# Kernel optimization log

Measured on AMD Instinct MI355X. Metric: run time of the kernel, lower is better.

The kernel has to match this reference:

```python
import jax, jax.numpy as jnp
import numpy as np
from jax import lax

N, L, LQ = 1024, 120, 30
V, D = 50000, 200
POSV, P = 201, 5
H, R = 230, 96
BAG = 8
B = N // BAG
EMB = 3 * D + 2 * P  # 610


def setup_inputs() -> dict:
    key = jax.random.key(0)
    k = jax.random.split(key, 14)
    X = jax.random.randint(k[0], (N, L), 0, V, dtype=jnp.int32)
    Q = jax.random.randint(k[1], (N, LQ), 0, V, dtype=jnp.int32)
    X_Pos1 = jax.random.randint(k[2], (N, L), 0, POSV, dtype=jnp.int32)
    X_Pos2 = jax.random.randint(k[3], (N, L), 0, POSV, dtype=jnp.int32)
    starts = jnp.arange(B, dtype=jnp.int32) * BAG
    X_Scope = jnp.stack([starts, starts + BAG], axis=1)  # [B,2] bag boundaries
    X_Rel = jax.random.randint(k[4], (B,), 0, R, dtype=jnp.int32)
    word_emb = jax.random.normal(k[5], (V, D), jnp.float32) * 0.02
    pos1_emb = jax.random.normal(k[6], (POSV, P), jnp.float32) * 0.02
    pos2_emb = jax.random.normal(k[7], (POSV, P), jnp.float32) * 0.02
    ws_w = jax.random.normal(k[8], (D,), jnp.float32) * 0.05
    wq_w = jax.random.normal(k[9], (D,), jnp.float32) * 0.05
    wsq_w = jax.random.normal(k[10], (D,), jnp.float32) * 0.05
    conv_w = jax.random.normal(k[11], (H, EMB, 3), jnp.float32) * 0.02
    rel_w = jax.random.normal(k[12], (R, H), jnp.float32) * 0.05
    return {
        'X': X, 'Q': Q, 'X_Pos1': X_Pos1, 'X_Pos2': X_Pos2,
        'X_Scope': X_Scope, 'X_Rel': X_Rel,
        'word_emb': word_emb, 'pos1_emb': pos1_emb, 'pos2_emb': pos2_emb,
        'ws_w': ws_w, 'ws_b': jnp.zeros((), jnp.float32),
        'wq_w': wq_w, 'wq_b': jnp.zeros((), jnp.float32),
        'wsq_w': wsq_w, 'wsq_b': jnp.zeros((), jnp.float32),
        'conv_w': conv_w, 'conv_b': jnp.zeros((H,), jnp.float32),
        'rel_w': rel_w, 'rel_b': jnp.zeros((R,), jnp.float32),
    }


def _forward(X, Q, X_Pos1, X_Pos2, X_Scope, X_Rel, word_emb, pos1_emb, pos2_emb,
             ws_w, ws_b, wq_w, wq_b, wsq_w, wsq_b, conv_w, conv_b, rel_w, rel_b):
    s = word_emb[X]            # [N,L,D]
    q = word_emb[Q]            # [N,LQ,D]
    p1 = pos1_emb[X_Pos1]      # [N,L,P]
    p2 = pos2_emb[X_Pos2]
    # ---- qs_att (BiDAF-style), vectorized over the original per-q-position loop ----
    sq = jnp.einsum('nld,nqd,d->nlq', s, q, wsq_w) + wsq_b            # [N,L,LQ]
    h = (s @ ws_w + ws_b)[:, :, None] + (q @ wq_w + wq_b)[:, None, :] + sq
    a = jax.nn.softmax(h, axis=2)
    s2q = jnp.einsum('nlq,nqd->nld', a, q)                            # s2q_att
    bvec = jax.nn.softmax(jnp.max(h, axis=2), axis=1)                 # [N,L]
    q2s = jnp.einsum('nl,nld->nd', bvec, s)[:, None, :]               # [N,1,D]
    x = jnp.concatenate([s, s * s2q, s * q2s], axis=-1)               # [N,L,3D]
    x = jnp.concatenate([x, p1, p2], axis=-1)                         # [N,L,EMB]
    # ---- CNN encoder: conv1d(k=3, same) -> max-over-time -> relu ----
    xc = lax.conv_general_dilated(x.transpose(0, 2, 1), conv_w, (1,), 'SAME',
                                  dimension_numbers=('NCH', 'OIH', 'NCH'))
    xc = xc + conv_b[None, :, None]
    feat = jax.nn.relu(jnp.max(xc, axis=2))                           # [N,H]
    # ---- bag self-attention: per-bag scaled dot-product over sentences ----
    bag_id = jnp.searchsorted(X_Scope[:, 1], jnp.arange(feat.shape[0]), side='right')
    same = bag_id[:, None] == bag_id[None, :]
    scores = (feat @ feat.T) / jnp.sqrt(jnp.float32(feat.shape[-1]))
    scores = jnp.where(same, scores, -1e30)
    feat = jax.nn.softmax(scores, axis=-1) @ feat                     # [N,H]
    # ---- selective attention with gold relation query (segment softmax) ----
    relq = rel_w[X_Rel]                                               # [B,H]
    z = jnp.einsum('nh,nh->n', feat, relq[bag_id])
    m = jax.ops.segment_max(z, bag_id, num_segments=B)
    e = jnp.exp(z - m[bag_id])
    denom = jax.ops.segment_sum(e, bag_id, num_segments=B)
    w = e / denom[bag_id]
    bag_rep = jax.ops.segment_sum(w[:, None] * feat, bag_id, num_segments=B)
    return bag_rep @ rel_w.T + rel_b                                  # [B,R]


def reference(X, Q, X_Pos1, X_Pos2, X_Scope, X_Rel, word_emb, pos1_emb, pos2_emb,
              ws_w, ws_b, wq_w, wq_b, wsq_w, wsq_b, conv_w, conv_b, rel_w, rel_b):
    return _forward(X, Q, X_Pos1, X_Pos2, X_Scope, X_Rel, word_emb, pos1_emb, pos2_emb,
                    ws_w, ws_b, wq_w, wq_b, wsq_w, wsq_b, conv_w, conv_b, rel_w, rel_b)
```

## Files before the change

kernel.cpp:

```cpp
#include <hip/hip_runtime.h>
#include <hip/hip_bf16.h>

#define N_    1024
#define L_    120
#define LQ_   30
#define D_    200
#define P_    5
#define H_    230
#define R_    96
#define BAG_  8
#define B_    128
#define EMB_  610
#define SROWS 130
#define SSTR  232
#define XSTR  72
#define NCH   21

typedef __hip_bfloat16 bf16;
typedef __attribute__((ext_vector_type(8))) short short8;
typedef __attribute__((ext_vector_type(4))) short short4_;
typedef __attribute__((ext_vector_type(4))) float f32x4;

__device__ __forceinline__ float wred_sum64(float v) {
#pragma unroll
  for (int m = 32; m; m >>= 1) v += __shfl_xor(v, m, 64);
  return v;
}
__device__ __forceinline__ float wred_max64(float v) {
#pragma unroll
  for (int m = 32; m; m >>= 1) v = fmaxf(v, __shfl_xor(v, m, 64));
  return v;
}
__device__ __forceinline__ short f2b(float f) {
  bf16 h = __float2bfloat16(f);
  return __builtin_bit_cast(short, h);
}
__device__ __forceinline__ float b2f(bf16 h) { return __bfloat162float(h); }

__global__ __launch_bounds__(256) void k0_prep_w(
    const float* __restrict__ conv_w, bf16* __restrict__ wt)
{
  const int idx = blockIdx.x * 256 + threadIdx.x;
  int e = idx & 7, lane = (idx >> 3) & 63;
  int fid = idx >> 9;
  int ni = fid & 15, cb = (fid >> 4) % NCH, k = fid / (NCH * 16);
  int h = ni * 16 + (lane & 15);
  int ccl = ((lane >> 4) << 3) + e;
  float v = 0.f;
  if (h < H_) {
    int emb_c = -1;
    if (cb < 7) {
      int d = cb * 32 + ccl;
      if (d < D_) emb_c = d;
    } else if (cb < 20) {
      int t = cb - 7;
      int d = 16 * t + (ccl & 15);
      if (d < D_) emb_c = (ccl < 16) ? (D_ + d) : (2 * D_ + d);
    } else if (ccl < 2 * P_) {
      emb_c = 3 * D_ + ccl;
    }
    if (emb_c >= 0) v = conv_w[(size_t)h * (EMB_ * 3) + emb_c * 3 + k];
  }
  wt[idx] = __float2bfloat16(v);
}

__global__ __launch_bounds__(1024, 4) void kf_fused(
    const int* __restrict__ X, const int* __restrict__ Q,
    const int* __restrict__ P1, const int* __restrict__ P2,
    const float* __restrict__ word_emb,
    const float* __restrict__ pos1_emb, const float* __restrict__ pos2_emb,
    const float* __restrict__ ws_w, const float* __restrict__ ws_b,
    const float* __restrict__ wq_w, const float* __restrict__ wq_b,
    const float* __restrict__ wsq_w,
    const bf16* __restrict__ wt, const float* __restrict__ conv_b,
    float* __restrict__ feat)
{
  const int n = blockIdx.x;
  const int tid = threadIdx.x;
  const int w = tid >> 6, lane = tid & 63;
  const int g = lane >> 4, c = lane & 15;
  const int wm = w >> 3;
  const int wn = w & 7;
  const int w8 = w & 7;

  __shared__ __align__(16) bf16 s_lds[SROWS][SSTR];
  __shared__ __align__(16) bf16 qT[208][40];
  __shared__ __align__(16) bf16 a_bf[128][40];
  __shared__ __align__(16) bf16 xstage[2][SROWS][XSTR];
  __shared__ __align__(16) bf16 pos_lds[L_][10];
  __shared__ float hred[16][32];
  __shared__ float wsv[D_], wqv[D_], wsqv[D_];
  __shared__ float sdot[128], qdot[32], hmax[128], bvec[L_];
  __shared__ float q2p[4][D_];
  __shared__ int xidxs[L_], qidxs[LQ_];

  bf16 (*qsw)[SSTR] = (bf16(*)[SSTR])&xstage[0][0][0];

  {
    const int4 z4 = {0, 0, 0, 0};
    for (int t = tid; t < SROWS * SSTR * 2 / 16; t += 1024) ((int4*)s_lds)[t] = z4;
    for (int t = tid; t < 208 * 40 * 2 / 16;     t += 1024) ((int4*)qT)[t] = z4;
    for (int t = tid; t < 32 * SSTR * 2 / 16;    t += 1024) ((int4*)qsw)[t] = z4;
  }
  if (tid < 2) qdot[30 + tid] = 0.f;
  if (tid >= 120 && tid < 128) sdot[tid] = 0.f;
  for (int t = tid; t < D_; t += 1024) { wsv[t] = ws_w[t]; wqv[t] = wq_w[t]; wsqv[t] = wsq_w[t]; }
  if (tid < L_) xidxs[tid] = X[n * L_ + tid];
  else if (tid >= 128 && tid < 128 + LQ_) qidxs[tid - 128] = Q[n * LQ_ + (tid - 128)];
  __syncthreads();

  const float wsb = ws_b[0], wqb = wq_b[0];

  for (int l = w; l < L_; l += 16) {
    const int idx = xidxs[l];
    if (lane < 50) {
      const int d = lane * 4;
      float4 v = *(const float4*)(word_emb + (size_t)idx * D_ + d);
      short4_ pk; pk.x = f2b(v.x); pk.y = f2b(v.y); pk.z = f2b(v.z); pk.w = f2b(v.w);
      *(short4_*)&s_lds[1 + l][d] = pk;
    }
  }
  for (int e = tid; e < L_ * 10; e += 1024) {
    int r = e / 10, p = e % 10;
    float v = (p < P_) ? pos1_emb[(size_t)P1[n * L_ + r] * P_ + p]
                       : pos2_emb[(size_t)P2[n * L_ + r] * P_ + (p - P_)];
    pos_lds[r][p] = __float2bfloat16(v);
  }
  for (int j = w; j < LQ_; j += 16) {
    const int idx = qidxs[j];
    float part = 0.f;
    if (lane < 50) {
      const int d = lane * 4;
      float4 v = *(const float4*)(word_emb + (size_t)idx * D_ + d);
      part = v.x * wqv[d] + v.y * wqv[d + 1] + v.z * wqv[d + 2] + v.w * wqv[d + 3];
      short4_ pk;
      pk.x = f2b(v.x * wsqv[d]);     pk.y = f2b(v.y * wsqv[d + 1]);
      pk.z = f2b(v.z * wsqv[d + 2]); pk.w = f2b(v.w * wsqv[d + 3]);
      *(short4_*)&qsw[j][d] = pk;
      qT[d][j]     = __float2bfloat16(v.x);
      qT[d + 1][j] = __float2bfloat16(v.y);
      qT[d + 2][j] = __float2bfloat16(v.z);
      qT[d + 3][j] = __float2bfloat16(v.w);
    }
    float sum = wred_sum64(part);
    if (lane == 0) qdot[j] = sum + wqb;
  }
  __syncthreads();

  f32x4 acc0 = {0.f, 0.f, 0.f, 0.f}, acc1 = {0.f, 0.f, 0.f, 0.f};
  if (w < 8) {
#pragma unroll
    for (int kk = 0; kk < 7; ++kk) {
      short8 af = *(const short8*)&s_lds[1 + 16 * w + c][kk * 32 + g * 8];
      short8 b0 = *(const short8*)&qsw[c][kk * 32 + g * 8];
      short8 b1 = *(const short8*)&qsw[16 + c][kk * 32 + g * 8];
      acc0 = __builtin_amdgcn_mfma_f32_16x16x32_bf16(af, b0, acc0, 0, 0, 0);
      acc1 = __builtin_amdgcn_mfma_f32_16x16x32_bf16(af, b1, acc1, 0, 0, 0);
    }
  } else {
    const int idx = tid - 512;
    if (idx < 480) {
      const int r = idx >> 2, base = (idx & 3) * 50;
      float a = 0.f;
#pragma unroll 5
      for (int i = 0; i < 50; i += 2) {
        a += b2f(s_lds[1 + r][base + i]) * wsv[base + i];
        a += b2f(s_lds[1 + r][base + i + 1]) * wsv[base + i + 1];
      }
      a += __shfl_xor(a, 1, 64);
      a += __shfl_xor(a, 2, 64);
      if ((idx & 3) == 0) sdot[r] = a + wsb;
    }
  }
  __syncthreads();

  if (w < 8) {
    const int rbase = 16 * w + 4 * g;
    const float qd0 = qdot[c], qd1 = qdot[16 + c];
#pragma unroll
    for (int reg = 0; reg < 4; ++reg) {
      const int r = rbase + reg;
      const float s0 = sdot[r];
      float h0 = acc0[reg] + s0 + qd0;
      float h1 = (c < 14) ? (acc1[reg] + s0 + qd1) : -1e30f;
      float m = fmaxf(h0, h1);
#pragma unroll
      for (int msk = 1; msk < 16; msk <<= 1) m = fmaxf(m, __shfl_xor(m, msk, 64));
      float e0 = expf(h0 - m);
      float e1 = (c < 14) ? expf(h1 - m) : 0.f;
      float ssum = e0 + e1;
#pragma unroll
      for (int msk = 1; msk < 16; msk <<= 1) ssum += __shfl_xor(ssum, msk, 64);
      float inv = 1.f / ssum;
      a_bf[r][c]      = __float2bfloat16(e0 * inv);
      a_bf[r][16 + c] = __float2bfloat16(e1 * inv);
      if (c == 0) hmax[r] = m;
    }
  } else {
    const int4 z4 = {0, 0, 0, 0};
    for (int t = tid - 512; t < 2 * SROWS * XSTR * 2 / 16; t += 512) ((int4*)xstage)[t] = z4;
  }
  __syncthreads();

  if (w == 0) {
    float v0 = hmax[lane];
    float v1 = (lane < L_ - 64) ? hmax[64 + lane] : -1e30f;
    float m = wred_max64(fmaxf(v0, v1));
    float e0 = expf(v0 - m);
    float e1 = (lane < L_ - 64) ? expf(v1 - m) : 0.f;
    float inv = 1.f / wred_sum64(e0 + e1);
    bvec[lane] = e0 * inv;
    if (lane < L_ - 64) bvec[64 + lane] = e1 * inv;
  }
  __syncthreads();

  {
    const int d = tid & 255, quarter = tid >> 8;
    if (d < D_) {
      const int lb = quarter * 30;
      float a0 = 0.f, a1 = 0.f;
      for (int l = 0; l < 30; l += 2) {
        a0 += bvec[lb + l]     * b2f(s_lds[1 + lb + l][d]);
        a1 += bvec[lb + l + 1] * b2f(s_lds[1 + lb + l + 1][d]);
      }
      q2p[quarter][d] = a0 + a1;
    }
  }
  __syncthreads();

  const short* wts = (const short*)wt;
  const short8 aft = *(const short8*)&a_bf[16 * w8 + c][g * 8];

  f32x4 acc[4][2];
#pragma unroll
  for (int i = 0; i < 4; ++i) {
    acc[i][0] = (f32x4){0.f, 0.f, 0.f, 0.f};
    acc[i][1] = (f32x4){0.f, 0.f, 0.f, 0.f};
  }

  for (int p = 0; p < 7; ++p) {
    {
      const int t = 2 * p + wm;
      bf16 (*buf)[XSTR] = xstage[p & 1];
      if (t < 13) {
        short8 bfr = *(const short8*)&qT[t * 16 + c][g * 8];
        f32x4 o = __builtin_amdgcn_mfma_f32_16x16x32_bf16(aft, bfr, (f32x4){0.f,0.f,0.f,0.f}, 0, 0, 0);
#pragma unroll
        for (int reg = 0; reg < 4; ++reg) {
          const int r = 16 * w8 + 4 * g + reg;
          if (r < L_) {
            float sv = b2f(s_lds[1 + r][t * 16 + c]);
            buf[1 + r][(t & 1) * 32 + c] = __float2bfloat16(sv * o[reg]);
          }
        }
        for (int e = tid & 511; e < L_ * 16; e += 512) {
          const int row = e >> 4, cc = e & 15, dd = t * 16 + cc;
          float v = (dd < D_)
              ? b2f(s_lds[1 + row][dd]) * (q2p[0][dd] + q2p[1][dd] + q2p[2][dd] + q2p[3][dd])
              : 0.f;
          buf[1 + row][(t & 1) * 32 + 16 + cc] = __float2bfloat16(v);
        }
      } else {
        for (int e = tid & 511; e < SROWS * 32; e += 512) {
          const int r = e >> 5, cc = e & 31;
          bf16 v = __float2bfloat16(0.f);
          if (r >= 1 && r <= L_ && cc < 2 * P_) v = pos_lds[r - 1][cc];
          buf[r][32 + cc] = v;
        }
      }
    }

#pragma unroll
    for (int k = 0; k < 3; ++k) {
      short8 bx0 = *(const short8*)(
          wts + (((size_t)((k * NCH + p) * 16 + wn * 2 + 0)) << 9) + lane * 8);
      short8 bx1 = *(const short8*)(
          wts + (((size_t)((k * NCH + p) * 16 + wn * 2 + 1)) << 9) + lane * 8);
#pragma unroll
      for (int mi = 0; mi < 4; ++mi) {
        short8 af = *(const short8*)&s_lds[wm * 64 + mi * 16 + c + k][p * 32 + g * 8];
        acc[mi][0] = __builtin_amdgcn_mfma_f32_16x16x32_bf16(af, bx0, acc[mi][0], 0, 0, 0);
        acc[mi][1] = __builtin_amdgcn_mfma_f32_16x16x32_bf16(af, bx1, acc[mi][1], 0, 0, 0);
      }
    }
    __syncthreads();

    {
      bf16 (*buf)[XSTR] = xstage[p & 1];
#pragma unroll
      for (int s2 = 0; s2 < 2; ++s2) {
        const int t = 2 * p + s2;
        const int cb = (t < 13) ? (7 + t) : 20;
#pragma unroll
        for (int k = 0; k < 3; ++k) {
          short8 bw0 = *(const short8*)(
              wts + (((size_t)((k * NCH + cb) * 16 + wn * 2 + 0)) << 9) + lane * 8);
          short8 bw1 = *(const short8*)(
              wts + (((size_t)((k * NCH + cb) * 16 + wn * 2 + 1)) << 9) + lane * 8);
#pragma unroll
          for (int mi = 0; mi < 4; ++mi) {
            short8 afx = *(const short8*)&buf[wm * 64 + mi * 16 + c + k][s2 * 32 + g * 8];
            acc[mi][0] = __builtin_amdgcn_mfma_f32_16x16x32_bf16(afx, bw0, acc[mi][0], 0, 0, 0);
            acc[mi][1] = __builtin_amdgcn_mfma_f32_16x16x32_bf16(afx, bw1, acc[mi][1], 0, 0, 0);
          }
        }
      }
    }
  }

  const int pbase = wm * 64 + (g << 2);
#pragma unroll
  for (int ni = 0; ni < 2; ++ni) {
    float m = -1e30f;
#pragma unroll
    for (int mi = 0; mi < 4; ++mi)
#pragma unroll
      for (int reg = 0; reg < 4; ++reg) {
        int pos = pbase + mi * 16 + reg;
        if (pos < L_) m = fmaxf(m, acc[mi][ni][reg]);
      }
    m = fmaxf(m, __shfl_xor(m, 16, 64));
    m = fmaxf(m, __shfl_xor(m, 32, 64));
    if (g == 0) hred[w][ni * 16 + c] = m;
  }
  __syncthreads();
  if (tid < H_) {
    const int wn2 = tid >> 5, x = tid & 31;
    float m = fmaxf(hred[wn2][x], hred[8 + wn2][x]);
    feat[(size_t)n * H_ + tid] = fmaxf(0.f, m + conv_b[tid]);
  }
}

__global__ __launch_bounds__(256) void k3_bag(
    const float* __restrict__ feat, const int* __restrict__ X_Rel,
    const float* __restrict__ rel_w, const float* __restrict__ rel_b,
    float* __restrict__ out)
{
  const int b = blockIdx.x;
  const int tid = threadIdx.x;
  __shared__ float f[BAG_][231];
  __shared__ float f2[BAG_][231];
  __shared__ float sc[BAG_][BAG_];
  __shared__ float relq[H_];
  __shared__ float zred[BAG_];
  __shared__ float wsel[BAG_];
  __shared__ float brep[H_];

  for (int t = tid; t < BAG_ * H_; t += 256) {
    int i = t / H_, h = t % H_;
    f[i][h] = feat[(size_t)(b * BAG_ + i) * H_ + h];
  }
  const int rel = X_Rel[b];
  for (int t = tid; t < H_; t += 256) relq[t] = rel_w[(size_t)rel * H_ + t];
  __syncthreads();

  if (tid < BAG_ * BAG_) {
    int i = tid >> 3, j = tid & 7;
    float acc = 0.f;
    for (int h = 0; h < H_; ++h) acc += f[i][h] * f[j][h];
    sc[i][j] = acc * (1.0f / sqrtf((float)H_));
  }
  __syncthreads();
  if (tid < BAG_) {
    float m = -1e30f;
    for (int j = 0; j < BAG_; ++j) m = fmaxf(m, sc[tid][j]);
    float s = 0.f;
    for (int j = 0; j < BAG_; ++j) { float e = expf(sc[tid][j] - m); sc[tid][j] = e; s += e; }
    float inv = 1.0f / s;
    for (int j = 0; j < BAG_; ++j) sc[tid][j] *= inv;
  }
  __syncthreads();
  for (int t = tid; t < BAG_ * H_; t += 256) {
    int i = t / H_, h = t % H_;
    float acc = 0.f;
#pragma unroll
    for (int j = 0; j < BAG_; ++j) acc += sc[i][j] * f[j][h];
    f2[i][h] = acc;
  }
  __syncthreads();
  if (tid < BAG_) {
    float acc = 0.f;
    for (int h = 0; h < H_; ++h) acc += f2[tid][h] * relq[h];
    zred[tid] = acc;
  }
  __syncthreads();
  if (tid == 0) {
    float m = -1e30f;
    for (int i = 0; i < BAG_; ++i) m = fmaxf(m, zred[i]);
    float s = 0.f;
    for (int i = 0; i < BAG_; ++i) { float e = expf(zred[i] - m); wsel[i] = e; s += e; }
    float inv = 1.0f / s;
    for (int i = 0; i < BAG_; ++i) wsel[i] *= inv;
  }
  __syncthreads();
  for (int t = tid; t < H_; t += 256) {
    float acc = 0.f;
#pragma unroll
    for (int i = 0; i < BAG_; ++i) acc += wsel[i] * f2[i][t];
    brep[t] = acc;
  }
  __syncthreads();
  if (tid < R_) {
    float acc = 0.f;
    for (int h = 0; h < H_; ++h) acc += brep[h] * rel_w[(size_t)tid * H_ + h];
    out[(size_t)b * R_ + tid] = acc + rel_b[tid];
  }
}

extern "C" void kernel_launch(void* const* d_in, const int* in_sizes, int n_in,
                              void* d_out, int out_size, void* d_ws, size_t ws_size,
                              hipStream_t stream)
{
  const int*   X        = (const int*)d_in[0];
  const int*   Q        = (const int*)d_in[1];
  const int*   P1       = (const int*)d_in[2];
  const int*   P2       = (const int*)d_in[3];
  const int*   X_Rel    = (const int*)d_in[5];
  const float* word_emb = (const float*)d_in[6];
  const float* pos1_emb = (const float*)d_in[7];
  const float* pos2_emb = (const float*)d_in[8];
  const float* ws_w     = (const float*)d_in[9];
  const float* ws_b     = (const float*)d_in[10];
  const float* wq_w     = (const float*)d_in[11];
  const float* wq_b     = (const float*)d_in[12];
  const float* wsq_w    = (const float*)d_in[13];
  const float* conv_w   = (const float*)d_in[15];
  const float* conv_b   = (const float*)d_in[16];
  const float* rel_w    = (const float*)d_in[17];
  const float* rel_b    = (const float*)d_in[18];

  const size_t feat_bytes = ((size_t)N_ * H_ * sizeof(float) + 255) & ~(size_t)255;
  float* feat = (float*)d_ws;
  bf16*  wt   = (bf16*)((char*)d_ws + feat_bytes);

  const int wt_elems = 3 * NCH * 16 * 64 * 8;
  k0_prep_w<<<wt_elems / 256, 256, 0, stream>>>(conv_w, wt);
  kf_fused<<<N_, 1024, 0, stream>>>(X, Q, P1, P2, word_emb, pos1_emb, pos2_emb,
                                    ws_w, ws_b, wq_w, wq_b, wsq_w, wt, conv_b, feat);
  k3_bag<<<B_, 256, 0, stream>>>(feat, X_Rel, rel_w, rel_b, (float*)d_out);
}
```

Before: 205.4 us.

## Reuse A fragments across conv taps with per-tap accumulators and shuffle-shift reduction

The convolution GEMM loaded a separate shifted A fragment from LDS for each of the three kernel taps. It now loads each A fragment once per chunk and keeps three separate accumulator sets, one per tap. The outputs are then combined by shifting rows through cross-lane shuffles, with the tile-boundary values passed between waves through new shared arrays. This cuts LDS reads to a third, but it triples the accumulator registers (96 floats), which risks register pressure and lower occupancy, and it adds an extra barrier.

Result: slower. 608.9 us (+196.5%).

```diff
diff --git a/kernel.cpp b/kernel.cpp
--- a/kernel.cpp
+++ b/kernel.cpp
@@ -89,6 +89,7 @@
   __shared__ __align__(16) bf16 xstage[2][SROWS][XSTR];
   __shared__ __align__(16) bf16 pos_lds[L_][10];
   __shared__ float hred[16][32];
+  __shared__ float exch0[8][32], exch2[8][32];
   __shared__ float wsv[D_], wqv[D_], wsqv[D_];
   __shared__ float sdot[128], qdot[32], hmax[128], bvec[L_];
   __shared__ float q2p[4][D_];
@@ -231,12 +232,14 @@
   const short* wts = (const short*)wt;
   const short8 aft = *(const short8*)&a_bf[16 * w8 + c][g * 8];
 
-  f32x4 acc[4][2];
-#pragma unroll
-  for (int i = 0; i < 4; ++i) {
-    acc[i][0] = (f32x4){0.f, 0.f, 0.f, 0.f};
-    acc[i][1] = (f32x4){0.f, 0.f, 0.f, 0.f};
-  }
+  f32x4 acc[3][4][2];
+#pragma unroll
+  for (int k = 0; k < 3; ++k)
+#pragma unroll
+    for (int i = 0; i < 4; ++i) {
+      acc[k][i][0] = (f32x4){0.f, 0.f, 0.f, 0.f};
+      acc[k][i][1] = (f32x4){0.f, 0.f, 0.f, 0.f};
+    }
 
   for (int p = 0; p < 7; ++p) {
     {
@@ -270,18 +273,22 @@
       }
     }
 
-#pragma unroll
-    for (int k = 0; k < 3; ++k) {
-      short8 bx0 = *(const short8*)(
-          wts + (((size_t)((k * NCH + p) * 16 + wn * 2 + 0)) << 9) + lane * 8);
-      short8 bx1 = *(const short8*)(
-          wts + (((size_t)((k * NCH + p) * 16 + wn * 2 + 1)) << 9) + lane * 8);
-#pragma unroll
-      for (int mi = 0; mi < 4; ++mi) {
-        short8 af = *(const short8*)&s_lds[wm * 64 + mi * 16 + c + k][p * 32 + g * 8];
-        acc[mi][0] = __builtin_amdgcn_mfma_f32_16x16x32_bf16(af, bx0, acc[mi][0], 0, 0, 0);
-        acc[mi][1] = __builtin_amdgcn_mfma_f32_16x16x32_bf16(af, bx1, acc[mi][1], 0, 0, 0);
-      }
+    {
+      short8 af0 = *(const short8*)&s_lds[1 + wm * 64 +  0 + c][p * 32 + g * 8];
+      short8 af1 = *(const short8*)&s_lds[1 + wm * 64 + 16 + c][p * 32 + g * 8];
+      short8 af2 = *(const short8*)&s_lds[1 + wm * 64 + 32 + c][p * 32 + g * 8];
+      short8 af3 = *(const short8*)&s_lds[1 + wm * 64 + 48 + c][p * 32 + g * 8];
+#pragma unroll
+      for (int k = 0; k < 3; ++k)
+#pragma unroll
+        for (int ni = 0; ni < 2; ++ni) {
+          const short8 bw = *(const short8*)(
+              wts + (((size_t)((k * NCH + p) * 16 + wn * 2 + ni)) << 9) + lane * 8);
+          acc[k][0][ni] = __builtin_amdgcn_mfma_f32_16x16x32_bf16(af0, bw, acc[k][0][ni], 0, 0, 0);
+          acc[k][1][ni] = __builtin_amdgcn_mfma_f32_16x16x32_bf16(af1, bw, acc[k][1][ni], 0, 0, 0);
+          acc[k][2][ni] = __builtin_amdgcn_mfma_f32_16x16x32_bf16(af2, bw, acc[k][2][ni], 0, 0, 0);
+          acc[k][3][ni] = __builtin_amdgcn_mfma_f32_16x16x32_bf16(af3, bw, acc[k][3][ni], 0, 0, 0);
+        }
     }
     __syncthreads();
 
@@ -291,34 +298,62 @@
       for (int s2 = 0; s2 < 2; ++s2) {
         const int t = 2 * p + s2;
         const int cb = (t < 13) ? (7 + t) : 20;
-#pragma unroll
-        for (int k = 0; k < 3; ++k) {
-          short8 bw0 = *(const short8*)(
-              wts + (((size_t)((k * NCH + cb) * 16 + wn * 2 + 0)) << 9) + lane * 8);
-          short8 bw1 = *(const short8*)(
-              wts + (((size_t)((k * NCH + cb) * 16 + wn * 2 + 1)) << 9) + lane * 8);
-#pragma unroll
-          for (int mi = 0; mi < 4; ++mi) {
-            short8 afx = *(const short8*)&buf[wm * 64 + mi * 16 + c + k][s2 * 32 + g * 8];
-            acc[mi][0] = __builtin_amdgcn_mfma_f32_16x16x32_bf16(afx, bw0, acc[mi][0], 0, 0, 0);
-            acc[mi][1] = __builtin_amdgcn_mfma_f32_16x16x32_bf16(afx, bw1, acc[mi][1], 0, 0, 0);
+        short8 ax0 = *(const short8*)&buf[1 + wm * 64 +  0 + c][s2 * 32 + g * 8];
+        short8 ax1 = *(const short8*)&buf[1 + wm * 64 + 16 + c][s2 * 32 + g * 8];
+        short8 ax2 = *(const short8*)&buf[1 + wm * 64 + 32 + c][s2 * 32 + g * 8];
+        short8 ax3 = *(const short8*)&buf[1 + wm * 64 + 48 + c][s2 * 32 + g * 8];
+#pragma unroll
+        for (int k = 0; k < 3; ++k)
+#pragma unroll
+          for (int ni = 0; ni < 2; ++ni) {
+            const short8 bw = *(const short8*)(
+                wts + (((size_t)((k * NCH + cb) * 16 + wn * 2 + ni)) << 9) + lane * 8);
+            acc[k][0][ni] = __builtin_amdgcn_mfma_f32_16x16x32_bf16(ax0, bw, acc[k][0][ni], 0, 0, 0);
+            acc[k][1][ni] = __builtin_amdgcn_mfma_f32_16x16x32_bf16(ax1, bw, acc[k][1][ni], 0, 0, 0);
+            acc[k][2][ni] = __builtin_amdgcn_mfma_f32_16x16x32_bf16(ax2, bw, acc[k][2][ni], 0, 0, 0);
+            acc[k][3][ni] = __builtin_amdgcn_mfma_f32_16x16x32_bf16(ax3, bw, acc[k][3][ni], 0, 0, 0);
           }
-        }
       }
     }
   }
 
+  if (wm == 0) {
+    if (g == 3) {
+      exch0[wn][c]      = acc[0][3][0][3];
+      exch0[wn][16 + c] = acc[0][3][1][3];
+    }
+  } else {
+    if (g == 0) {
+      exch2[wn][c]      = acc[2][0][0][0];
+      exch2[wn][16 + c] = acc[2][0][1][0];
+    }
+  }
+  __syncthreads();
+
   const int pbase = wm * 64 + (g << 2);
 #pragma unroll
   for (int ni = 0; ni < 2; ++ni) {
+    const float bnd0 = (wm == 1) ? exch0[wn][ni * 16 + c] : 0.f;
+    const float bnd2 = (wm == 0) ? exch2[wn][ni * 16 + c] : 0.f;
     float m = -1e30f;
 #pragma unroll
-    for (int mi = 0; mi < 4; ++mi)
-#pragma unroll
-      for (int reg = 0; reg < 4; ++reg) {
-        int pos = pbase + mi * 16 + reg;
-        if (pos < L_) m = fmaxf(m, acc[mi][ni][reg]);
-      }
+    for (int mi = 0; mi < 4; ++mi) {
+      float aUp = __shfl(acc[0][mi][ni][3], (lane - 16) & 63, 64);
+      float aPrev = (mi > 0) ? __shfl(acc[0][mi - 1][ni][3], (lane + 48) & 63, 64) : bnd0;
+      float prev3 = (g >= 1) ? aUp : aPrev;
+      float aDn = __shfl(acc[2][mi][ni][0], (lane + 16) & 63, 64);
+      float aNext = (mi < 3) ? __shfl(acc[2][mi + 1][ni][0], (lane - 48) & 63, 64) : bnd2;
+      float next0 = (g <= 2) ? aDn : aNext;
+      float v0 = prev3             + acc[1][mi][ni][0] + acc[2][mi][ni][1];
+      float v1 = acc[0][mi][ni][0] + acc[1][mi][ni][1] + acc[2][mi][ni][2];
+      float v2 = acc[0][mi][ni][1] + acc[1][mi][ni][2] + acc[2][mi][ni][3];
+      float v3 = acc[0][mi][ni][2] + acc[1][mi][ni][3] + next0;
+      const int p0 = pbase + mi * 16;
+      if (p0     < L_) m = fmaxf(m, v0);
+      if (p0 + 1 < L_) m = fmaxf(m, v1);
+      if (p0 + 2 < L_) m = fmaxf(m, v2);
+      if (p0 + 3 < L_) m = fmaxf(m, v3);
+    }
     m = fmaxf(m, __shfl_xor(m, 16, 64));
     m = fmaxf(m, __shfl_xor(m, 32, 64));
     if (g == 0) hred[w][ni * 16 + c] = m;
```
